# Kernel tuning notes

Hardware: AMD Instinct MI355X
Metric: run time of the kernel (lower is better)

Reference implementation:

```python
import jax, jax.numpy as jnp
import numpy as np

NUM_HEADS = 8
LATENT_FRAME = 4
D_MODEL = 1024
D_FF = 1024  # dim_feedforward == output_dim in the torch module
N_LAYERS = 6
IN_DIM = 128
LN_EPS = 1e-5


def get_slopes(n):
    # standard ALiBi slopes for power-of-two head counts: 2^{-8(i+1)/n}
    return jnp.asarray([2.0 ** (-8.0 * (i + 1) / n) for i in range(n)], jnp.float32)


def alibi_mask(num_heads, T):
    # non-causal ('future') ALiBi: additive bias -slope_h * |i - j|, shape (H, T, T)
    dist = jnp.abs(jnp.arange(T)[:, None] - jnp.arange(T)[None, :]).astype(jnp.float32)
    return -get_slopes(num_heads)[:, None, None] * dist


def layernorm(x, g, b):
    m = jnp.mean(x, axis=-1, keepdims=True)
    v = jnp.mean((x - m) ** 2, axis=-1, keepdims=True)
    return (x - m) * jax.lax.rsqrt(v + LN_EPS) * g + b


def encoder_layer(x, p, mask):
    # torch TransformerEncoderLayer, post-norm, gelu(exact), dropout=0
    B, T, D = x.shape
    H, Dh = NUM_HEADS, D // NUM_HEADS
    qkv = x @ p['in_w'].T + p['in_b']                      # (B,T,3D)
    q, k, v = jnp.split(qkv, 3, axis=-1)
    hsplit = lambda t: t.reshape(B, T, H, Dh).transpose(0, 2, 1, 3)  # (B,H,T,Dh)
    q, k, v = hsplit(q), hsplit(k), hsplit(v)
    scores = jnp.einsum('bhqd,bhkd->bhqk', q, k) / float(np.sqrt(Dh)) + mask[None]
    attn = jax.nn.softmax(scores, axis=-1)
    o = jnp.einsum('bhqk,bhkd->bhqd', attn, v).transpose(0, 2, 1, 3).reshape(B, T, D)
    o = o @ p['out_w'].T + p['out_b']
    x = layernorm(x + o, p['ln1_g'], p['ln1_b'])
    ff = jax.nn.gelu(x @ p['ff1_w'].T + p['ff1_b'], approximate=False) @ p['ff2_w'].T + p['ff2_b']
    return layernorm(x + ff, p['ln2_g'], p['ln2_b'])


def setup_inputs() -> dict:
    key = jax.random.key(0)
    ks = iter(jax.random.split(key, 32))
    s = 0.02
    B, T, F = 8, 2048, IN_DIM
    Fs = F * LATENT_FRAME  # 512
    inp = {
        'x': jax.random.normal(next(ks), (B, T, F), jnp.float32),
        'pre_w': jax.random.normal(next(ks), (D_MODEL, Fs), jnp.float32) * s,
        'pre_b': jnp.zeros((D_MODEL,), jnp.float32),
        'in_w': jax.random.normal(next(ks), (N_LAYERS, 3 * D_MODEL, D_MODEL), jnp.float32) * s,
        'in_b': jnp.zeros((N_LAYERS, 3 * D_MODEL), jnp.float32),
        'out_w': jax.random.normal(next(ks), (N_LAYERS, D_MODEL, D_MODEL), jnp.float32) * s,
        'out_b': jnp.zeros((N_LAYERS, D_MODEL), jnp.float32),
        'ln1_g': jnp.ones((N_LAYERS, D_MODEL), jnp.float32),
        'ln1_b': jnp.zeros((N_LAYERS, D_MODEL), jnp.float32),
        'ff1_w': jax.random.normal(next(ks), (N_LAYERS, D_FF, D_MODEL), jnp.float32) * s,
        'ff1_b': jnp.zeros((N_LAYERS, D_FF), jnp.float32),
        'ff2_w': jax.random.normal(next(ks), (N_LAYERS, D_MODEL, D_FF), jnp.float32) * s,
        'ff2_b': jnp.zeros((N_LAYERS, D_MODEL), jnp.float32),
        'ln2_g': jnp.ones((N_LAYERS, D_MODEL), jnp.float32),
        'ln2_b': jnp.zeros((N_LAYERS, D_MODEL), jnp.float32),
        'post_w': jax.random.normal(next(ks), (D_MODEL, D_MODEL), jnp.float32) * s,
        'post_b': jnp.zeros((D_MODEL,), jnp.float32),
    }
    return inp


def reference(x, pre_w, pre_b, in_w, in_b, out_w, out_b, ln1_g, ln1_b,
              ff1_w, ff1_b, ff2_w, ff2_b, ln2_g, ln2_b, post_w, post_b):
    B, T, F = x.shape
    Tl = T // LATENT_FRAME
    x = x.reshape(B, Tl, F * LATENT_FRAME)
    x = x @ pre_w.T + pre_b                     # (B, Tl, D)
    mask = alibi_mask(NUM_HEADS, Tl)            # (H, Tl, Tl), shared by all batches
    layers = dict(in_w=in_w, in_b=in_b, out_w=out_w, out_b=out_b,
                  ln1_g=ln1_g, ln1_b=ln1_b, ff1_w=ff1_w, ff1_b=ff1_b,
                  ff2_w=ff2_w, ff2_b=ff2_b, ln2_g=ln2_g, ln2_b=ln2_b)
    def step(h, p):
        return encoder_layer(h, p, mask), None
    x, _ = jax.lax.scan(step, x, layers)
    return x @ post_w.T + post_b
```

## Files before the change

### kernel.cpp

```cpp
#include <hip/hip_runtime.h>
#include <hip/hip_bf16.h>

#define B 8
#define TL 512
#define M_ROWS 4096
#define D 1024
#define DFF 1024
#define H 8
#define DH 128
#define NL 6

typedef unsigned short ushort_t;
typedef unsigned int uint_t;
typedef short bf16x8 __attribute__((ext_vector_type(8)));
typedef float f32x4 __attribute__((ext_vector_type(4)));

__device__ __forceinline__ ushort_t f2bf(float f) {
    uint_t u = __float_as_uint(f);
    u += 0x7FFFu + ((u >> 16) & 1u);
    return (ushort_t)(u >> 16);
}
__device__ __forceinline__ float gelu_exact(float x) {
    return 0.5f * x * (1.0f + erff(x * 0.70710678118654752f));
}
__device__ __forceinline__ void gload_lds16(const ushort_t* g, ushort_t* l) {
    __builtin_amdgcn_global_load_lds(
        (const __attribute__((address_space(1))) void*)g,
        (__attribute__((address_space(3))) void*)l, 16, 0, 0);
}

struct CvtArgs {
    const float* s[7];
    ushort_t* d[7];
    int nq[7];
    int bstart[8];
};

__global__ __launch_bounds__(256) void cvt_all(CvtArgs a) {
    const int bid = blockIdx.x;
#pragma unroll
    for (int seg = 0; seg < 7; ++seg) {
        const int b0 = a.bstart[seg], b1 = a.bstart[seg + 1];
        if (bid < b0 || bid >= b1) continue;
        const int stride = (b1 - b0) * 256;
        const float* s = a.s[seg];
        ushort_t* d = a.d[seg];
        const int nq = a.nq[seg];
        for (int i = (bid - b0) * 256 + threadIdx.x; i < nq; i += stride) {
            float4 v = *(const float4*)(s + (size_t)i * 4);
            ushort4 o;
            o.x = f2bf(v.x); o.y = f2bf(v.y); o.z = f2bf(v.z); o.w = f2bf(v.w);
            *(ushort4*)(d + (size_t)i * 4) = o;
        }
    }
}

#define LSLOT64(r, c) (((r) * 8 + ((c) ^ ((r) & 7))) * 8)

__global__ __launch_bounds__(256) void gemm_n64(
    const ushort_t* __restrict__ A, const ushort_t* __restrict__ W,
    const float* __restrict__ bias, float* __restrict__ Cf,
    ushort_t* __restrict__ Cb, int M, int N, int K, int do_gelu) {
    __shared__ ushort_t As[128 * 64];
    __shared__ ushort_t Bs[64 * 64];

    const int tid = threadIdx.x;
    const int lane = tid & 63;
    const int w = tid >> 6;
    const int wm = (w & 2) * 32;
    const int wn = (w & 1) * 32;
    const int bm = blockIdx.y * 128;
    const int bn = blockIdx.x * 64;

    const ushort_t* gA[4];
    ushort_t* lA[4];
#pragma unroll
    for (int t = 0; t < 4; ++t) {
        int s = tid + t * 256;
        int r = s >> 3, gl = (s & 7) ^ (r & 7);
        gA[t] = A + (size_t)(bm + r) * K + gl * 8;
        lA[t] = &As[s * 8];
    }
    const ushort_t* gB[2];
    ushort_t* lB[2];
#pragma unroll
    for (int t = 0; t < 2; ++t) {
        int s = tid + t * 256;
        int r = s >> 3, gl = (s & 7) ^ (r & 7);
        gB[t] = W + (size_t)(bn + r) * K + gl * 8;
        lB[t] = &Bs[s * 8];
    }

    const int fr = lane & 15;
    const int fq = lane >> 4;
    int aoff[4][2], boff[2][2];
#pragma unroll
    for (int t = 0; t < 4; ++t)
#pragma unroll
        for (int s = 0; s < 2; ++s)
            aoff[t][s] = LSLOT64(wm + t * 16 + fr, s * 4 + fq);
#pragma unroll
    for (int t = 0; t < 2; ++t)
#pragma unroll
        for (int s = 0; s < 2; ++s)
            boff[t][s] = LSLOT64(wn + t * 16 + fr, s * 4 + fq);

    f32x4 acc[4][2];
#pragma unroll
    for (int i = 0; i < 4; ++i)
#pragma unroll
        for (int j = 0; j < 2; ++j) acc[i][j] = (f32x4){0.f, 0.f, 0.f, 0.f};

    for (int k0 = 0; k0 < K; k0 += 64) {
#pragma unroll
        for (int t = 0; t < 4; ++t) gload_lds16(gA[t] + k0, lA[t]);
#pragma unroll
        for (int t = 0; t < 2; ++t) gload_lds16(gB[t] + k0, lB[t]);
        __syncthreads();

#pragma unroll
        for (int s = 0; s < 2; ++s) {
            bf16x8 af[4], bf[2];
#pragma unroll
            for (int t = 0; t < 4; ++t) af[t] = *(const bf16x8*)&As[aoff[t][s]];
#pragma unroll
            for (int t = 0; t < 2; ++t) bf[t] = *(const bf16x8*)&Bs[boff[t][s]];
#pragma unroll
            for (int i = 0; i < 4; ++i)
#pragma unroll
                for (int j = 0; j < 2; ++j)
                    acc[i][j] = __builtin_amdgcn_mfma_f32_16x16x32_bf16(
                        af[i], bf[j], acc[i][j], 0, 0, 0);
        }
        __syncthreads();
    }

#pragma unroll
    for (int tj = 0; tj < 2; ++tj) {
        const int n = bn + wn + tj * 16 + fr;
        const float bv = bias[n];
#pragma unroll
        for (int ti = 0; ti < 4; ++ti) {
            const int m0 = bm + wm + ti * 16 + fq * 4;
            f32x4 a = acc[ti][tj];
#pragma unroll
            for (int r = 0; r < 4; ++r) {
                float v = a[r] + bv;
                if (do_gelu) v = gelu_exact(v);
                const size_t off = (size_t)(m0 + r) * N + n;
                if (Cf) Cf[off] = v;
                if (Cb) Cb[off] = f2bf(v);
            }
        }
    }
}

#define QPHASE(par, mh, nh, LOADA, ...)                                        \
    {                                                                          \
        if (LOADA) {                                                           \
            _Pragma("unroll") for (int im = 0; im < 4; ++im)                   \
                _Pragma("unroll") for (int ks = 0; ks < 2; ++ks)               \
                    af[im][ks] = *(const bf16x8*)&AsB[(par)*16384 +            \
                                                     (mh)*8192 + aoff[im][ks]];\
        }                                                                      \
        _Pragma("unroll") for (int jn = 0; jn < 2; ++jn)                       \
            _Pragma("unroll") for (int ks = 0; ks < 2; ++ks)                   \
                bfv[jn][ks] = *(const bf16x8*)&BsB[(par)*16384 +               \
                                                  (nh)*8192 + boff[jn][ks]];   \
        __VA_ARGS__;                                                           \
        __builtin_amdgcn_s_barrier();                                          \
        asm volatile("s_waitcnt lgkmcnt(0)" ::: "memory");                     \
        __builtin_amdgcn_sched_barrier(0);                                     \
        __builtin_amdgcn_s_setprio(1);                                         \
        _Pragma("unroll") for (int im = 0; im < 4; ++im)                       \
            _Pragma("unroll") for (int jn = 0; jn < 2; ++jn)                   \
                _Pragma("unroll") for (int ks = 0; ks < 2; ++ks)               \
                    acc[(mh)*4 + im][(nh)*2 + jn] =                            \
                        __builtin_amdgcn_mfma_f32_16x16x32_bf16(               \
                            af[im][ks], bfv[jn][ks],                           \
                            acc[(mh)*4 + im][(nh)*2 + jn], 0, 0, 0);           \
        __builtin_amdgcn_s_setprio(0);                                         \
        asm volatile("s_waitcnt vmcnt(4)" ::: "memory");                       \
        __builtin_amdgcn_s_barrier();                                          \
    }

__global__ __launch_bounds__(512, 2) void gemm_qkv256(
    const ushort_t* __restrict__ A, const ushort_t* __restrict__ W,
    const float* __restrict__ bias, ushort_t* __restrict__ Qb,
    ushort_t* __restrict__ Kb, ushort_t* __restrict__ Vt) {
    extern __shared__ ushort_t lds[];
    ushort_t* AsB = lds;
    ushort_t* BsB = lds + 32768;
    const int K = 1024;

    const int bid = blockIdx.x;
    const int wg = (bid & 7) * 24 + (bid >> 3);
    const int by = wg / 12, bx = wg - by * 12;
    const int bm = by * 256, bn = bx * 256;

    const int tid = threadIdx.x;
    const int lane = tid & 63;
    const int w = tid >> 6;
    const int wm = w >> 2;
    const int wn = w & 3;
    const int fr = lane & 15;
    const int fq = lane >> 4;

    const ushort_t* gA[2];
    const ushort_t* gB[2];
    int sdst[2];
#pragma unroll
    for (int u = 0; u < 2; ++u) {
        int s = tid + u * 512;
        int r = s >> 3, c = (s & 7) ^ (r & 7);
        gA[u] = A + (size_t)(bm + r) * K + c * 8;
        gB[u] = W + (size_t)(bn + r) * K + c * 8;
        sdst[u] = s * 8;
    }

    int aoff[4][2], boff[2][2];
#pragma unroll
    for (int im = 0; im < 4; ++im)
#pragma unroll
        for (int ks = 0; ks < 2; ++ks)
            aoff[im][ks] = LSLOT64(wm * 64 + im * 16 + fr, ks * 4 + fq);
#pragma unroll
    for (int jn = 0; jn < 2; ++jn)
#pragma unroll
        for (int ks = 0; ks < 2; ++ks)
            boff[jn][ks] = LSLOT64(wn * 32 + jn * 16 + fr, ks * 4 + fq);

    f32x4 acc[8][4];
#pragma unroll
    for (int i = 0; i < 8; ++i)
#pragma unroll
        for (int j = 0; j < 4; ++j) acc[i][j] = (f32x4){0.f, 0.f, 0.f, 0.f};

    auto stageA = [&](int p, int h, int tk) {
#pragma unroll
        for (int u = 0; u < 2; ++u)
            gload_lds16(gA[u] + (size_t)h * 128 * K + tk * 64,
                        &AsB[p * 16384 + h * 8192 + sdst[u]]);
    };
    auto stageB = [&](int p, int h, int tk) {
#pragma unroll
        for (int u = 0; u < 2; ++u)
            gload_lds16(gB[u] + (size_t)h * 128 * K + tk * 64,
                        &BsB[p * 16384 + h * 8192 + sdst[u]]);
    };

    stageA(0, 0, 0); stageB(0, 0, 0); stageB(0, 1, 0); stageA(0, 1, 0);
    asm volatile("s_waitcnt vmcnt(0)" ::: "memory");
    __builtin_amdgcn_s_barrier();

    bf16x8 af[4][2], bfv[2][2];

#pragma unroll 1
    for (int it = 0; it < 8; ++it) {
        const int t0 = 2 * it;
        QPHASE(0, 0, 0, 1, { stageA(1, 0, t0 + 1); })
        QPHASE(0, 0, 1, 0, { stageB(1, 0, t0 + 1); })
        QPHASE(0, 1, 0, 1, { stageB(1, 1, t0 + 1); })
        QPHASE(0, 1, 1, 0, { stageA(1, 1, t0 + 1); })
        const bool st = (it < 7);
        QPHASE(1, 0, 0, 1, { if (st) stageA(0, 0, t0 + 2); })
        QPHASE(1, 0, 1, 0, { if (st) stageB(0, 0, t0 + 2); })
        QPHASE(1, 1, 0, 1, { if (st) stageB(0, 1, t0 + 2); })
        QPHASE(1, 1, 1, 0, { if (st) stageA(0, 1, t0 + 2); })
    }

    const float qscale = 0.08838834764831845f;
#pragma unroll
    for (int j = 0; j < 4; ++j) {
        const int n = bn + (j >> 1) * 128 + wn * 32 + (j & 1) * 16 + fr;
        const float bv = bias[n];
#pragma unroll
        for (int i = 0; i < 8; ++i) {
            const int m0 = bm + (i >> 2) * 128 + wm * 64 + (i & 3) * 16 + fq * 4;
            f32x4 a = acc[i][j];
            if (n < D) {
#pragma unroll
                for (int r = 0; r < 4; ++r)
                    Qb[(size_t)(m0 + r) * D + n] = f2bf((a[r] + bv) * qscale);
            } else if (n < 2 * D) {
#pragma unroll
                for (int r = 0; r < 4; ++r)
                    Kb[(size_t)(m0 + r) * D + (n - D)] = f2bf(a[r] + bv);
            } else {
                const int h = (n - 2 * D) >> 7;
                const int dh = (n - 2 * D) & 127;
                const int bb = m0 >> 9;
                const int t = m0 & 511;
                ushort4 pk;
                pk.x = f2bf(a[0] + bv); pk.y = f2bf(a[1] + bv);
                pk.z = f2bf(a[2] + bv); pk.w = f2bf(a[3] + bv);
                *(ushort4*)&Vt[((size_t)(bb * H + h) * DH + dh) * TL + t] = pk;
            }
        }
    }
}

#define LSW16(r, g) ((((r) << 4) + ((g) ^ ((r) & 7))) << 3)
#define LSW8(r, g) ((((r) << 3) + ((g) ^ ((r) & 7))) << 3)

__global__ __launch_bounds__(256, 2) void attn_mfma(
    const ushort_t* __restrict__ Qb, const ushort_t* __restrict__ Kb,
    const ushort_t* __restrict__ Vt, ushort_t* __restrict__ Ab) {
    __shared__ ushort_t Qs[64 * 128];
    __shared__ ushort_t Ks[64 * 128];
    __shared__ ushort_t Vts[128 * 64];
    __shared__ ushort_t Ps[64 * 72];

    const int q0 = blockIdx.x * 64;
    const int bh = blockIdx.y;
    const int b = bh >> 3;
    const int h = bh & 7;
    const int tid = threadIdx.x;
    const int lane = tid & 63;
    const int w = tid >> 6;
    const int fr = lane & 15;
    const int fq = lane >> 4;

    const float slope = exp2f(-(float)(h + 1));

#pragma unroll
    for (int kk = 0; kk < 4; ++kk) {
        int s = tid + kk * 256;
        int r = s >> 4, gp = s & 15, gl = gp ^ (r & 7);
        gload_lds16(Qb + (size_t)(b * TL + q0 + r) * D + h * DH + gl * 8,
                    &Qs[s * 8]);
    }

    f32x4 o8[8];
    float m_i[4], l_i[4];
#pragma unroll
    for (int nt = 0; nt < 8; ++nt) o8[nt] = (f32x4){0.f, 0.f, 0.f, 0.f};
#pragma unroll
    for (int r = 0; r < 4; ++r) { m_i[r] = -1e30f; l_i[r] = 0.f; }

    for (int kt = 0; kt < TL / 64; ++kt) {
        __syncthreads();
#pragma unroll
        for (int kk = 0; kk < 4; ++kk) {
            int s = tid + kk * 256;
            int r = s >> 4, gp = s & 15, gl = gp ^ (r & 7);
            gload_lds16(Kb + (size_t)(b * TL + kt * 64 + r) * D + h * DH + gl * 8,
                        &Ks[s * 8]);
        }
#pragma unroll
        for (int kk = 0; kk < 4; ++kk) {
            int s = tid + kk * 256;
            int r = s >> 3, gp = s & 7, gl = gp ^ (r & 7);
            gload_lds16(Vt + ((size_t)bh * DH + r) * TL + kt * 64 + gl * 8,
                        &Vts[s * 8]);
        }
        __syncthreads();

        f32x4 sacc[4];
#pragma unroll
        for (int jt = 0; jt < 4; ++jt) sacc[jt] = (f32x4){0.f, 0.f, 0.f, 0.f};
#pragma unroll
        for (int s4 = 0; s4 < 4; ++s4) {
            bf16x8 aq = *(const bf16x8*)&Qs[LSW16(w * 16 + fr, s4 * 4 + fq)];
#pragma unroll
            for (int jt = 0; jt < 4; ++jt) {
                bf16x8 kb = *(const bf16x8*)&Ks[LSW16(jt * 16 + fr, s4 * 4 + fq)];
                sacc[jt] = __builtin_amdgcn_mfma_f32_16x16x32_bf16(
                    aq, kb, sacc[jt], 0, 0, 0);
            }
        }

        const int iq = q0 + w * 16 + fq * 4;
        const int jk = kt * 64 + fr;
        float al[4];
#pragma unroll
        for (int r = 0; r < 4; ++r) {
            float sv[4];
#pragma unroll
            for (int jt = 0; jt < 4; ++jt)
                sv[jt] = sacc[jt][r] -
                         slope * fabsf((float)(iq + r - jk - jt * 16));
            float mx = fmaxf(fmaxf(sv[0], sv[1]), fmaxf(sv[2], sv[3]));
            mx = fmaxf(mx, __shfl_xor(mx, 1));
            mx = fmaxf(mx, __shfl_xor(mx, 2));
            mx = fmaxf(mx, __shfl_xor(mx, 4));
            mx = fmaxf(mx, __shfl_xor(mx, 8));
            float mnew = fmaxf(m_i[r], mx);
            al[r] = __expf(m_i[r] - mnew);
            float rs = 0.f;
#pragma unroll
            for (int jt = 0; jt < 4; ++jt) {
                sv[jt] = __expf(sv[jt] - mnew);
                rs += sv[jt];
            }
            rs += __shfl_xor(rs, 1);
            rs += __shfl_xor(rs, 2);
            rs += __shfl_xor(rs, 4);
            rs += __shfl_xor(rs, 8);
            l_i[r] = l_i[r] * al[r] + rs;
            m_i[r] = mnew;
            const int prow = w * 16 + fq * 4 + r;
#pragma unroll
            for (int jt = 0; jt < 4; ++jt)
                Ps[prow * 72 + jt * 16 + fr] = f2bf(sv[jt]);
        }
#pragma unroll
        for (int nt = 0; nt < 8; ++nt)
#pragma unroll
            for (int r = 0; r < 4; ++r) o8[nt][r] *= al[r];

#pragma unroll
        for (int s2 = 0; s2 < 2; ++s2) {
            bf16x8 pa = *(const bf16x8*)&Ps[(w * 16 + fr) * 72 + s2 * 32 + fq * 8];
#pragma unroll
            for (int nt = 0; nt < 8; ++nt) {
                bf16x8 vb = *(const bf16x8*)&Vts[LSW8(nt * 16 + fr, s2 * 4 + fq)];
                o8[nt] = __builtin_amdgcn_mfma_f32_16x16x32_bf16(
                    pa, vb, o8[nt], 0, 0, 0);
            }
        }
    }

#pragma unroll
    for (int r = 0; r < 4; ++r) {
        float inv = 1.f / l_i[r];
        const size_t base = (size_t)(b * TL + q0 + w * 16 + fq * 4 + r) * D + h * DH;
#pragma unroll
        for (int nt = 0; nt < 8; ++nt)
            Ab[base + nt * 16 + fr] = f2bf(o8[nt][r] * inv);
    }
}

__global__ __launch_bounds__(256) void add_ln(const float* __restrict__ x,
                                              const float* __restrict__ y,
                                              const float* __restrict__ g,
                                              const float* __restrict__ bta,
                                              float* __restrict__ out,
                                              ushort_t* __restrict__ outb) {
    const int row = blockIdx.x * 4 + (threadIdx.x >> 6);
    const int lane = threadIdx.x & 63;
    const size_t rbase = (size_t)row * D;

    float4 v[4];
#pragma unroll
    for (int j = 0; j < 4; ++j) {
        float4 xv = *(const float4*)(x + rbase + lane * 4 + j * 256);
        float4 yv = *(const float4*)(y + rbase + lane * 4 + j * 256);
        v[j].x = xv.x + yv.x; v[j].y = xv.y + yv.y;
        v[j].z = xv.z + yv.z; v[j].w = xv.w + yv.w;
    }

    float s = 0.f;
#pragma unroll
    for (int j = 0; j < 4; ++j) s += v[j].x + v[j].y + v[j].z + v[j].w;
#pragma unroll
    for (int off = 32; off; off >>= 1) s += __shfl_xor(s, off);
    const float mean = s * (1.f / (float)D);

    float sq = 0.f;
#pragma unroll
    for (int j = 0; j < 4; ++j) {
        float d0 = v[j].x - mean, d1 = v[j].y - mean;
        float d2 = v[j].z - mean, d3 = v[j].w - mean;
        sq += d0 * d0 + d1 * d1 + d2 * d2 + d3 * d3;
    }
#pragma unroll
    for (int off = 32; off; off >>= 1) sq += __shfl_xor(sq, off);
    const float var = sq * (1.f / (float)D);
    const float inv = rsqrtf(var + 1e-5f);

#pragma unroll
    for (int j = 0; j < 4; ++j) {
        const int col = lane * 4 + j * 256;
        float4 gv = *(const float4*)(g + col);
        float4 bv = *(const float4*)(bta + col);
        float4 o;
        o.x = (v[j].x - mean) * inv * gv.x + bv.x;
        o.y = (v[j].y - mean) * inv * gv.y + bv.y;
        o.z = (v[j].z - mean) * inv * gv.z + bv.z;
        o.w = (v[j].w - mean) * inv * gv.w + bv.w;
        *(float4*)(out + rbase + col) = o;
        ushort4 ob;
        ob.x = f2bf(o.x); ob.y = f2bf(o.y); ob.z = f2bf(o.z); ob.w = f2bf(o.w);
        *(ushort4*)(outb + rbase + col) = ob;
    }
}

extern "C" void kernel_launch(void* const* d_in, const int* in_sizes, int n_in,
                              void* d_out, int out_size, void* d_ws, size_t ws_size,
                              hipStream_t stream) {
    const float* x_in   = (const float*)d_in[0];
    const float* pre_w  = (const float*)d_in[1];
    const float* pre_b  = (const float*)d_in[2];
    const float* in_w   = (const float*)d_in[3];
    const float* in_b   = (const float*)d_in[4];
    const float* out_w  = (const float*)d_in[5];
    const float* out_b  = (const float*)d_in[6];
    const float* ln1_g  = (const float*)d_in[7];
    const float* ln1_b  = (const float*)d_in[8];
    const float* ff1_w  = (const float*)d_in[9];
    const float* ff1_b  = (const float*)d_in[10];
    const float* ff2_w  = (const float*)d_in[11];
    const float* ff2_b  = (const float*)d_in[12];
    const float* ln2_g  = (const float*)d_in[13];
    const float* ln2_b  = (const float*)d_in[14];
    const float* post_w = (const float*)d_in[15];
    const float* post_b = (const float*)d_in[16];

    static bool attr_set = false;
    if (!attr_set) {
        hipFuncSetAttribute((const void*)gemm_qkv256,
                            hipFuncAttributeMaxDynamicSharedMemorySize, 131072);
        attr_set = true;
    }

    float* X = (float*)d_ws;
    float* Y = X + (size_t)M_ROWS * D;
    ushort_t* Xb   = (ushort_t*)(Y + (size_t)M_ROWS * D);
    ushort_t* Ab   = Xb + (size_t)M_ROWS * D;
    ushort_t* Qb   = Ab + (size_t)M_ROWS * D;
    ushort_t* Kb   = Qb + (size_t)M_ROWS * D;
    ushort_t* Vt   = Kb + (size_t)M_ROWS * D;
    ushort_t* xinb = Vt + (size_t)M_ROWS * D;
    ushort_t* pwb  = xinb + (size_t)M_ROWS * 512;
    ushort_t* iwb  = pwb + (size_t)D * 512;
    ushort_t* owb  = iwb + (size_t)NL * 3 * D * D;
    ushort_t* f1wb = owb + (size_t)NL * D * D;
    ushort_t* f2wb = f1wb + (size_t)NL * DFF * D;
    ushort_t* powb = f2wb + (size_t)NL * D * DFF;

    const dim3 blk(256);

    CvtArgs ca;
    ca.s[0] = x_in;   ca.d[0] = xinb; ca.nq[0] = (M_ROWS * 512) / 4;
    ca.s[1] = pre_w;  ca.d[1] = pwb;  ca.nq[1] = (D * 512) / 4;
    ca.s[2] = in_w;   ca.d[2] = iwb;  ca.nq[2] = (NL * 3 * D * D) / 4;
    ca.s[3] = out_w;  ca.d[3] = owb;  ca.nq[3] = (NL * D * D) / 4;
    ca.s[4] = ff1_w;  ca.d[4] = f1wb; ca.nq[4] = (NL * DFF * D) / 4;
    ca.s[5] = ff2_w;  ca.d[5] = f2wb; ca.nq[5] = (NL * D * DFF) / 4;
    ca.s[6] = post_w; ca.d[6] = powb; ca.nq[6] = (D * D) / 4;
    {
        long long total = 0;
        for (int i = 0; i < 7; ++i) total += ca.nq[i];
        long long cum = 0;
        ca.bstart[0] = 0;
        for (int i = 0; i < 7; ++i) {
            cum += ca.nq[i];
            ca.bstart[i + 1] = (int)((cum * 4096) / total);
        }
        ca.bstart[7] = 4096;
    }
    cvt_all<<<4096, blk, 0, stream>>>(ca);

    const dim3 gN64(D / 64, M_ROWS / 128);

    gemm_n64<<<gN64, blk, 0, stream>>>(xinb, pwb, pre_b, X, Xb,
                                       M_ROWS, D, 512, 0);

    for (int l = 0; l < NL; ++l) {
        gemm_qkv256<<<dim3(192), dim3(512), 131072, stream>>>(
            Xb, iwb + (size_t)l * 3 * D * D, in_b + (size_t)l * 3 * D,
            Qb, Kb, Vt);
        attn_mfma<<<dim3(TL / 64, B * H), blk, 0, stream>>>(Qb, Kb, Vt, Ab);
        gemm_n64<<<gN64, blk, 0, stream>>>(Ab, owb + (size_t)l * D * D,
                                           out_b + (size_t)l * D, Y, nullptr,
                                           M_ROWS, D, D, 0);
        add_ln<<<dim3(M_ROWS / 4), blk, 0, stream>>>(X, Y, ln1_g + (size_t)l * D,
                                                     ln1_b + (size_t)l * D, X, Xb);
        gemm_n64<<<gN64, blk, 0, stream>>>(Xb, f1wb + (size_t)l * DFF * D,
                                           ff1_b + (size_t)l * DFF, nullptr, Ab,
                                           M_ROWS, DFF, D, 1);
        gemm_n64<<<gN64, blk, 0, stream>>>(Ab, f2wb + (size_t)l * D * DFF,
                                           ff2_b + (size_t)l * D, Y, nullptr,
                                           M_ROWS, D, DFF, 0);
        add_ln<<<dim3(M_ROWS / 4), blk, 0, stream>>>(X, Y, ln2_g + (size_t)l * D,
                                                     ln2_b + (size_t)l * D, X, Xb);
    }

    gemm_n64<<<gN64, blk, 0, stream>>>(Xb, powb, post_b, (float*)d_out, nullptr,
                                       M_ROWS, D, D, 0);
}
```

Before: 1.131 ms.

## Double-buffer projection GEMMs with 128x128 tiles and LDS-staged coalesced epilogue

Replaces the 128x64 single-buffered projection GEMM with a 128x128-tile, 8-wave kernel that double-buffers its global-to-LDS loads, so the next K tile loads while the current one computes. The epilogue writes results through LDS and then emits float4/ushort4 row-contiguous stores instead of scattered scalar stores. The attention kernel also raises wave priority around its MFMA blocks. In exchange the grid is halved to one block per CU and LDS use grows to 64KB per block, which may reduce latency hiding.

```diff
diff --git a/kernel.cpp b/kernel.cpp
--- a/kernel.cpp
+++ b/kernel.cpp
@@ -57,53 +57,45 @@
 
 #define LSLOT64(r, c) (((r) * 8 + ((c) ^ ((r) & 7))) * 8)
 
-__global__ __launch_bounds__(256) void gemm_n64(
+__global__ __launch_bounds__(512) void gemm_n128(
     const ushort_t* __restrict__ A, const ushort_t* __restrict__ W,
     const float* __restrict__ bias, float* __restrict__ Cf,
     ushort_t* __restrict__ Cb, int M, int N, int K, int do_gelu) {
-    __shared__ ushort_t As[128 * 64];
-    __shared__ ushort_t Bs[64 * 64];
+    extern __shared__ ushort_t lds[];
 
     const int tid = threadIdx.x;
     const int lane = tid & 63;
     const int w = tid >> 6;
-    const int wm = (w & 2) * 32;
-    const int wn = (w & 1) * 32;
+    const int wm = w >> 2;
+    const int wn = w & 3;
     const int bm = blockIdx.y * 128;
-    const int bn = blockIdx.x * 64;
-
-    const ushort_t* gA[4];
-    ushort_t* lA[4];
-#pragma unroll
-    for (int t = 0; t < 4; ++t) {
-        int s = tid + t * 256;
-        int r = s >> 3, gl = (s & 7) ^ (r & 7);
-        gA[t] = A + (size_t)(bm + r) * K + gl * 8;
-        lA[t] = &As[s * 8];
-    }
-    const ushort_t* gB[2];
-    ushort_t* lB[2];
-#pragma unroll
-    for (int t = 0; t < 2; ++t) {
-        int s = tid + t * 256;
-        int r = s >> 3, gl = (s & 7) ^ (r & 7);
-        gB[t] = W + (size_t)(bn + r) * K + gl * 8;
-        lB[t] = &Bs[s * 8];
-    }
-
+    const int bn = blockIdx.x * 128;
     const int fr = lane & 15;
     const int fq = lane >> 4;
+
+    const ushort_t* gA[2];
+    const ushort_t* gB[2];
+    int sdst[2];
+#pragma unroll
+    for (int u = 0; u < 2; ++u) {
+        int s = tid + u * 512;
+        int r = s >> 3, c = (s & 7) ^ (r & 7);
+        gA[u] = A + (size_t)(bm + r) * K + c * 8;
+        gB[u] = W + (size_t)(bn + r) * K + c * 8;
+        sdst[u] = s * 8;
+    }
+
     int aoff[4][2], boff[2][2];
 #pragma unroll
-    for (int t = 0; t < 4; ++t)
-#pragma unroll
-        for (int s = 0; s < 2; ++s)
-            aoff[t][s] = LSLOT64(wm + t * 16 + fr, s * 4 + fq);
-#pragma unroll
-    for (int t = 0; t < 2; ++t)
-#pragma unroll
-        for (int s = 0; s < 2; ++s)
-            boff[t][s] = LSLOT64(wn + t * 16 + fr, s * 4 + fq);
+    for (int ti = 0; ti < 4; ++ti)
+#pragma unroll
+        for (int ks = 0; ks < 2; ++ks)
+            aoff[ti][ks] = LSLOT64(wm * 64 + ti * 16 + fr, ks * 4 + fq);
+#pragma unroll
+    for (int tj = 0; tj < 2; ++tj)
+#pragma unroll
+        for (int ks = 0; ks < 2; ++ks)
+            boff[tj][ks] = LSLOT64(wn * 32 + tj * 16 + fr, ks * 4 + fq);
 
     f32x4 acc[4][2];
 #pragma unroll
@@ -111,45 +103,78 @@
 #pragma unroll
         for (int j = 0; j < 2; ++j) acc[i][j] = (f32x4){0.f, 0.f, 0.f, 0.f};
 
-    for (int k0 = 0; k0 < K; k0 += 64) {
-#pragma unroll
-        for (int t = 0; t < 4; ++t) gload_lds16(gA[t] + k0, lA[t]);
-#pragma unroll
-        for (int t = 0; t < 2; ++t) gload_lds16(gB[t] + k0, lB[t]);
-        __syncthreads();
-
-#pragma unroll
-        for (int s = 0; s < 2; ++s) {
-            bf16x8 af[4], bf[2];
-#pragma unroll
-            for (int t = 0; t < 4; ++t) af[t] = *(const bf16x8*)&As[aoff[t][s]];
-#pragma unroll
-            for (int t = 0; t < 2; ++t) bf[t] = *(const bf16x8*)&Bs[boff[t][s]];
+    auto stage = [&](int buf, int k0) {
+#pragma unroll
+        for (int u = 0; u < 2; ++u)
+            gload_lds16(gA[u] + k0, &lds[buf * 8192 + sdst[u]]);
+#pragma unroll
+        for (int u = 0; u < 2; ++u)
+            gload_lds16(gB[u] + k0, &lds[16384 + buf * 8192 + sdst[u]]);
+    };
+    auto comp = [&](int buf) {
+#pragma unroll
+        for (int ks = 0; ks < 2; ++ks) {
+            bf16x8 af[4], bfv[2];
+#pragma unroll
+            for (int ti = 0; ti < 4; ++ti)
+                af[ti] = *(const bf16x8*)&lds[buf * 8192 + aoff[ti][ks]];
+#pragma unroll
+            for (int tj = 0; tj < 2; ++tj)
+                bfv[tj] = *(const bf16x8*)&lds[16384 + buf * 8192 + boff[tj][ks]];
 #pragma unroll
             for (int i = 0; i < 4; ++i)
 #pragma unroll
                 for (int j = 0; j < 2; ++j)
                     acc[i][j] = __builtin_amdgcn_mfma_f32_16x16x32_bf16(
-                        af[i], bf[j], acc[i][j], 0, 0, 0);
-        }
+                        af[i], bfv[j], acc[i][j], 0, 0, 0);
+        }
+    };
+
+    const int NT = K >> 6;
+    stage(0, 0);
+    __syncthreads();
+    int buf = 0;
+    for (int t = 0; t < NT; ++t) {
+        if (t + 1 < NT) stage(buf ^ 1, (t + 1) * 64);
+        comp(buf);
         __syncthreads();
-    }
-
-#pragma unroll
-    for (int tj = 0; tj < 2; ++tj) {
-        const int n = bn + wn + tj * 16 + fr;
-        const float bv = bias[n];
-#pragma unroll
-        for (int ti = 0; ti < 4; ++ti) {
-            const int m0 = bm + wm + ti * 16 + fq * 4;
-            f32x4 a = acc[ti][tj];
-#pragma unroll
-            for (int r = 0; r < 4; ++r) {
-                float v = a[r] + bv;
-                if (do_gelu) v = gelu_exact(v);
-                const size_t off = (size_t)(m0 + r) * N + n;
-                if (Cf) Cf[off] = v;
-                if (Cb) Cb[off] = f2bf(v);
+        buf ^= 1;
+    }
+
+    float bv[2];
+#pragma unroll
+    for (int tj = 0; tj < 2; ++tj) bv[tj] = bias[bn + wn * 32 + tj * 16 + fr];
+
+    float* eps = (float*)lds;
+#pragma unroll
+    for (int p = 0; p < 2; ++p) {
+        if (p) __syncthreads();
+        if (wm == p) {
+#pragma unroll
+            for (int ti = 0; ti < 4; ++ti)
+#pragma unroll
+                for (int tj = 0; tj < 2; ++tj)
+#pragma unroll
+                    for (int r = 0; r < 4; ++r) {
+                        float v = acc[ti][tj][r] + bv[tj];
+                        if (do_gelu) v = gelu_exact(v);
+                        eps[(ti * 16 + fq * 4 + r) * 132 +
+                            wn * 32 + tj * 16 + fr] = v;
+                    }
+        }
+        __syncthreads();
+#pragma unroll
+        for (int k = 0; k < 4; ++k) {
+            int f = tid + k * 512;
+            int row = f >> 5, c4 = f & 31;
+            float4 v = *(const float4*)&eps[row * 132 + c4 * 4];
+            const size_t off = (size_t)(bm + p * 64 + row) * N + bn + c4 * 4;
+            if (Cf) *(float4*)(Cf + off) = v;
+            if (Cb) {
+                ushort4 ob;
+                ob.x = f2bf(v.x); ob.y = f2bf(v.y);
+                ob.z = f2bf(v.z); ob.w = f2bf(v.w);
+                *(ushort4*)(Cb + off) = ob;
             }
         }
     }
@@ -359,6 +384,7 @@
         f32x4 sacc[4];
 #pragma unroll
         for (int jt = 0; jt < 4; ++jt) sacc[jt] = (f32x4){0.f, 0.f, 0.f, 0.f};
+        __builtin_amdgcn_s_setprio(1);
 #pragma unroll
         for (int s4 = 0; s4 < 4; ++s4) {
             bf16x8 aq = *(const bf16x8*)&Qs[LSW16(w * 16 + fr, s4 * 4 + fq)];
@@ -369,6 +395,7 @@
                     aq, kb, sacc[jt], 0, 0, 0);
             }
         }
+        __builtin_amdgcn_s_setprio(0);
 
         const int iq = q0 + w * 16 + fq * 4;
         const int jk = kt * 64 + fr;
@@ -409,6 +436,7 @@
 #pragma unroll
             for (int r = 0; r < 4; ++r) o8[nt][r] *= al[r];
 
+        __builtin_amdgcn_s_setprio(1);
 #pragma unroll
         for (int s2 = 0; s2 < 2; ++s2) {
             bf16x8 pa = *(const bf16x8*)&Ps[(w * 16 + fr) * 72 + s2 * 32 + fq * 8];
@@ -419,6 +447,7 @@
                     pa, vb, o8[nt], 0, 0, 0);
             }
         }
+        __builtin_amdgcn_s_setprio(0);
     }
 
 #pragma unroll
@@ -511,6 +540,8 @@
     if (!attr_set) {
         hipFuncSetAttribute((const void*)gemm_qkv256,
                             hipFuncAttributeMaxDynamicSharedMemorySize, 131072);
+        hipFuncSetAttribute((const void*)gemm_n128,
+                            hipFuncAttributeMaxDynamicSharedMemorySize, 65536);
         attr_set = true;
     }
 
@@ -552,31 +583,32 @@
     }
     cvt_all<<<4096, blk, 0, stream>>>(ca);
 
-    const dim3 gN64(D / 64, M_ROWS / 128);
-
-    gemm_n64<<<gN64, blk, 0, stream>>>(xinb, pwb, pre_b, X, Xb,
-                                       M_ROWS, D, 512, 0);
+    const dim3 gN128(D / 128, M_ROWS / 128);
+
+    gemm_n128<<<gN128, dim3(512), 65536, stream>>>(xinb, pwb, pre_b, X, Xb,
+                                                   M_ROWS, D, 512, 0);
 
     for (int l = 0; l < NL; ++l) {
         gemm_qkv256<<<dim3(192), dim3(512), 131072, stream>>>(
             Xb, iwb + (size_t)l * 3 * D * D, in_b + (size_t)l * 3 * D,
             Qb, Kb, Vt);
         attn_mfma<<<dim3(TL / 64, B * H), blk, 0, stream>>>(Qb, Kb, Vt, Ab);
-        gemm_n64<<<gN64, blk, 0, stream>>>(Ab, owb + (size_t)l * D * D,
-                                           out_b + (size_t)l * D, Y, nullptr,
-                                           M_ROWS, D, D, 0);
+        gemm_n128<<<gN128, dim3(512), 65536, stream>>>(
+            Ab, owb + (size_t)l * D * D, out_b + (size_t)l * D, Y, nullptr,
+            M_ROWS, D, D, 0);
         add_ln<<<dim3(M_ROWS / 4), blk, 0, stream>>>(X, Y, ln1_g + (size_t)l * D,
                                                      ln1_b + (size_t)l * D, X, Xb);
-        gemm_n64<<<gN64, blk, 0, stream>>>(Xb, f1wb + (size_t)l * DFF * D,
-                                           ff1_b + (size_t)l * DFF, nullptr, Ab,
-                                           M_ROWS, DFF, D, 1);
-        gemm_n64<<<gN64, blk, 0, stream>>>(Ab, f2wb + (size_t)l * D * DFF,
-                                           ff2_b + (size_t)l * D, Y, nullptr,
-                                           M_ROWS, D, DFF, 0);
+        gemm_n128<<<gN128, dim3(512), 65536, stream>>>(
+            Xb, f1wb + (size_t)l * DFF * D, ff1_b + (size_t)l * DFF, nullptr, Ab,
+            M_ROWS, DFF, D, 1);
+        gemm_n128<<<gN128, dim3(512), 65536, stream>>>(
+            Ab, f2wb + (size_t)l * D * DFF, ff2_b + (size_t)l * D, Y, nullptr,
+            M_ROWS, D, DFF, 0);
         add_ln<<<dim3(M_ROWS / 4), blk, 0, stream>>>(X, Y, ln2_g + (size_t)l * D,
                                                      ln2_b + (size_t)l * D, X, Xb);
     }
 
-    gemm_n64<<<gN64, blk, 0, stream>>>(Xb, powb, post_b, (float*)d_out, nullptr,
-                                       M_ROWS, D, D, 0);
-}
+    gemm_n128<<<gN128, dim3(512), 65536, stream>>>(Xb, powb, post_b,
+                                                   (float*)d_out, nullptr,
+                                                   M_ROWS, D, D, 0);
+}
```

Measured after the change: 1.127 ms. No clear change (-0.4%).
